# Kernel optimization log

Measured on AMD Instinct MI355X. Metric: run time of the kernel, lower is better.

The kernel has to match this reference:

```python
import jax, jax.numpy as jnp
import numpy as np

KQ_D = 64  # head dim from init_kwargs

def setup_inputs() -> dict:
    key = jax.random.key(0)
    k1, k2, k3, k4 = jax.random.split(key, 4)
    B, H, S, D = 2, 12, 2048, KQ_D
    q = jax.random.normal(k1, (B, H, S, D), dtype=jnp.float32)
    k = jax.random.normal(k2, (B, H, S, D), dtype=jnp.float32)
    v = jax.random.normal(k3, (B, H, S, D), dtype=jnp.float32)
    mask = jax.random.randint(k4, (B, 1, S, S), 0, 2, dtype=jnp.int32)
    return {"q": q, "k": k, "v": v, "mask": mask}

def reference(q, k, v, mask):
    # attn = (q @ k^T) / sqrt(kq_d)
    scale = 1.0 / (KQ_D ** 0.5)
    attn = jnp.einsum('bhqd,bhkd->bhqk', q, k) * scale
    # masked_fill(mask == 0, -1e9)
    attn = jnp.where(mask == 0, jnp.float32(-1e9), attn)
    # softmax over keys; dropout is identity in eval/reference mode
    attn = jax.nn.softmax(attn, axis=-1)
    out = jnp.einsum('bhqk,bhkd->bhqd', attn, v)
    return out
```

## Files before the change

### kernel.cpp

```cpp
#include <hip/hip_runtime.h>
#include <hip/hip_bf16.h>

#define S_LEN 2048
#define D_DIM 64
#define NH    12
#define NB    2
#define BH_N  (NB*NH)
#define TILES 32
#define TILE_BYTES 16384
#define KV_WS_BYTES ((size_t)BH_N * TILES * TILE_BYTES)
#define MASK_WORDS  ((size_t)NB * S_LEN * TILES)
#define WS_NEEDED   (KV_WS_BYTES + MASK_WORDS * 8)

typedef __attribute__((ext_vector_type(8))) short short8;
typedef __attribute__((ext_vector_type(4))) float f32x4;

static __device__ inline unsigned bfbits(float f) {
    __hip_bfloat16 h = __float2bfloat16(f);
    return (unsigned)*reinterpret_cast<const unsigned short*>(&h);
}

static __device__ inline unsigned bfpack2(float a, float b) {
    __hip_bfloat162 h = __float22bfloat162_rn(make_float2(a, b));
    return *reinterpret_cast<const unsigned*>(&h);
}

static __device__ inline void gload_lds16(const void* g, unsigned ldsoff) {
    __builtin_amdgcn_global_load_lds(
        (__attribute__((address_space(1))) void*)(unsigned long long)(uintptr_t)g,
        (__attribute__((address_space(3))) void*)(unsigned long long)ldsoff,
        16, 0, 0);
}

__global__ __launch_bounds__(256) void prep(const float* __restrict__ k,
                                            const float* __restrict__ v,
                                            const int* __restrict__ mask,
                                            char* __restrict__ wsKV,
                                            unsigned long long* __restrict__ wm) {
    __shared__ __align__(16) float sv[64 * 68];
    const int tid = threadIdx.x;
    const int bid = blockIdx.x;
    if (bid < 768) {
        const int t = bid & 31, bh = bid >> 5;
        const int kv0 = t * 64;
        const float* kb = k + (size_t)bh * (S_LEN * D_DIM);
        const float* vb = v + (size_t)bh * (S_LEN * D_DIM);
        char* img = wsKV + ((size_t)bh * TILES + t) * TILE_BYTES;

#pragma unroll
        for (int g = 0; g < 4; ++g) {
            int i = g * 256 + tid;
            int row = i >> 4, cb = (i & 15) << 3;
            int cp = cb ^ ((row & 7) << 4);
            float4 f = *(const float4*)(kb + (size_t)(kv0 + row) * D_DIM + (cp >> 1));
            uint2 u;
            u.x = bfpack2(f.x, f.y);
            u.y = bfpack2(f.z, f.w);
            *(uint2*)(img + (size_t)i * 8) = u;
            float4 fv = *(const float4*)(vb + (size_t)(kv0 + row) * D_DIM + ((i & 15) << 2));
            *(float4*)&sv[row * 68 + ((i & 15) << 2)] = fv;
        }
        __syncthreads();
#pragma unroll
        for (int g = 0; g < 4; ++g) {
            int i = g * 256 + tid;
            int drow = i >> 4, cb = (i & 15) << 3;
            int cp = cb ^ ((drow & 7) << 4);
            int key0 = cp >> 1;
            uint2 u;
            u.x = bfpack2(sv[(key0 + 0) * 68 + drow], sv[(key0 + 1) * 68 + drow]);
            u.y = bfpack2(sv[(key0 + 2) * 68 + drow], sv[(key0 + 3) * 68 + drow]);
            *(uint2*)(img + 8192 + (size_t)i * 8) = u;
        }
    } else {
        const int lane = tid & 63;
        const int wgid = (bid - 768) * 4 + (tid >> 6);
#pragma unroll 1
        for (int g = 0; g < 16; ++g) {
            const int t0 = wgid * 64 + g * 4;
            const size_t base = (size_t)t0 * 64 + lane;
            int m0 = mask[base];
            int m1 = mask[base + 64];
            int m2 = mask[base + 128];
            int m3 = mask[base + 192];
            unsigned long long b0 = __ballot(m0 != 0);
            unsigned long long b1 = __ballot(m1 != 0);
            unsigned long long b2 = __ballot(m2 != 0);
            unsigned long long b3 = __ballot(m3 != 0);
            if (lane == 0) {
                wm[t0 + 0] = b0; wm[t0 + 1] = b1;
                wm[t0 + 2] = b2; wm[t0 + 3] = b3;
            }
        }
    }
}

__global__ __launch_bounds__(256, 3) void attn_main(
    const float* __restrict__ q, const char* __restrict__ wsKV,
    const unsigned long long* __restrict__ wm, float* __restrict__ out)
{
    __shared__ __align__(16) char smem[2 * TILE_BYTES + 8192];

    const int tid  = threadIdx.x;
    const int wave = tid >> 6;
    const int lane = tid & 63;
    const int l16  = lane & 15;
    const int lhi  = lane >> 4;

    const int f  = blockIdx.x;
    const int n  = (f & 7) * 96 + (f >> 3);
    const int bx = n & 31;
    const int bh = n >> 5;
    const int b  = bh / NH;
    const int qw = bx * 64 + wave * 16;
    const int qq = qw + l16;

    const float* qb = q + (size_t)bh * (S_LEN * D_DIM);
    float*       ob = out + (size_t)bh * (S_LEN * D_DIM);
    const char*  tileBase = wsKV + (size_t)bh * TILES * TILE_BYTES;
    const size_t widx = ((size_t)b * S_LEN + qq) * TILES;

    const float PRE = 0.125f * 1.44269504088896f;

    short8 bq[2];
#pragma unroll
    for (int ks = 0; ks < 2; ++ks) {
        const float* src = qb + (size_t)qq * D_DIM + ks * 32 + lhi * 8;
        float4 f0 = *(const float4*)(src);
        float4 f1 = *(const float4*)(src + 4);
        short8 a;
        a[0] = (short)bfbits(f0.x * PRE); a[1] = (short)bfbits(f0.y * PRE);
        a[2] = (short)bfbits(f0.z * PRE); a[3] = (short)bfbits(f0.w * PRE);
        a[4] = (short)bfbits(f1.x * PRE); a[5] = (short)bfbits(f1.y * PRE);
        a[6] = (short)bfbits(f1.z * PRE); a[7] = (short)bfbits(f1.w * PRE);
        bq[ks] = a;
    }

    f32x4 o[4];
#pragma unroll
    for (int dt = 0; dt < 4; ++dt) o[dt] = (f32x4){0.f, 0.f, 0.f, 0.f};
    float lsum = 0.f;

    const unsigned smem_base = (unsigned)(uintptr_t)(&smem[0]);
    char* pw = smem + 2 * TILE_BYTES + wave * 2048;

    unsigned long long mw = wm[widx];
#pragma unroll
    for (int j = 0; j < 4; ++j) {
        unsigned off = (unsigned)(wave * 4096 + j * 1024 + lane * 16);
        gload_lds16(tileBase + off, smem_base + off);
    }
    __syncthreads();

    int buf = 0;
    for (int t = 0; t < 32; ++t) {
        if (t < 31) {
            const char* timg = tileBase + (size_t)(t + 1) * TILE_BYTES;
            unsigned dstb = smem_base + (unsigned)((buf ^ 1) * TILE_BYTES);
#pragma unroll
            for (int j = 0; j < 4; ++j) {
                unsigned off = (unsigned)(wave * 4096 + j * 1024 + lane * 16);
                gload_lds16(timg + off, dstb + off);
            }
        }
        unsigned long long mw_next = (t < 31) ? wm[widx + t + 1] : 0ull;

        const char* sK  = smem + buf * TILE_BYTES;
        const char* sVt = sK + 8192;

        f32x4 sc[4];
#pragma unroll
        for (int tt = 0; tt < 4; ++tt) sc[tt] = (f32x4){0.f, 0.f, 0.f, 0.f};
#pragma unroll
        for (int ks = 0; ks < 2; ++ks) {
#pragma unroll
            for (int tt = 0; tt < 4; ++tt) {
                int row = tt * 16 + l16;
                int byte = row * 128 + ((ks * 64 + lhi * 16) ^ ((row & 7) << 4));
                short8 ak = *(const short8*)(sK + byte);
                sc[tt] = __builtin_amdgcn_mfma_f32_16x16x32_bf16(ak, bq[ks], sc[tt], 0, 0, 0);
            }
        }

        short8 bvv[2][4];
#pragma unroll
        for (int ks = 0; ks < 2; ++ks)
#pragma unroll
            for (int dt = 0; dt < 4; ++dt) {
                int drow = dt * 16 + l16;
                int vbyte = drow * 128 + ((ks * 64 + lhi * 16) ^ ((drow & 7) << 4));
                bvv[ks][dt] = *(const short8*)(sVt + vbyte);
            }

        float rs = 0.f;
#pragma unroll
        for (int tt = 0; tt < 4; ++tt) {
            unsigned nib = (unsigned)(mw >> (tt * 16 + lhi * 4)) & 0xFu;
#pragma unroll
            for (int r = 0; r < 4; ++r) {
                float s = ((nib >> r) & 1u) ? sc[tt][r] : -1e9f;
                float p = exp2f(s);
                sc[tt][r] = p;
                rs += p;
            }
        }
        lsum += rs;

#pragma unroll
        for (int tt = 0; tt < 4; ++tt) {
            uint2 u;
            u.x = bfpack2(sc[tt][0], sc[tt][1]);
            u.y = bfpack2(sc[tt][2], sc[tt][3]);
            int byte = l16 * 128 + (((tt * 16 + lhi * 4) * 2) ^ ((l16 & 7) << 4));
            *(uint2*)(pw + byte) = u;
        }

#pragma unroll
        for (int ks = 0; ks < 2; ++ks) {
            int pbyte = l16 * 128 + ((ks * 64 + lhi * 16) ^ ((l16 & 7) << 4));
            short8 pa = *(const short8*)(pw + pbyte);
#pragma unroll
            for (int dt = 0; dt < 4; ++dt)
                o[dt] = __builtin_amdgcn_mfma_f32_16x16x32_bf16(pa, bvv[ks][dt], o[dt], 0, 0, 0);
        }

        __syncthreads();
        buf ^= 1;
        mw = mw_next;
    }

    lsum += __shfl_xor(lsum, 16);
    lsum += __shfl_xor(lsum, 32);
    float invl = 1.0f / lsum;
    float ir[4];
#pragma unroll
    for (int r = 0; r < 4; ++r) ir[r] = __shfl(invl, lhi * 4 + r);
#pragma unroll
    for (int dt = 0; dt < 4; ++dt)
#pragma unroll
        for (int r = 0; r < 4; ++r) {
            int qrow = qw + lhi * 4 + r;
            int dcol = dt * 16 + l16;
            ob[(size_t)qrow * D_DIM + dcol] = o[dt][r] * ir[r];
        }
}

__global__ __launch_bounds__(256, 3) void attn_fallback(
    const float* __restrict__ q, const float* __restrict__ k,
    const float* __restrict__ v, const int* __restrict__ mask,
    float* __restrict__ out)
{
    __shared__ __align__(16) unsigned short sK[4096];
    __shared__ __align__(16) unsigned short sVt[4096];
    __shared__ __align__(16) unsigned short sP[4096];

    const int tid  = threadIdx.x;
    const int wave = tid >> 6;
    const int lane = tid & 63;
    const int l16  = lane & 15;
    const int lhi  = lane >> 4;

    const int bh = blockIdx.y;
    const int b  = bh / NH;
    const int q0 = blockIdx.x * 64;
    const int qw = q0 + wave * 16;
    const int qq = qw + l16;

    const float* qbase = q + (size_t)bh * S_LEN * D_DIM;
    const float* kbase = k + (size_t)bh * S_LEN * D_DIM;
    const float* vbase = v + (size_t)bh * S_LEN * D_DIM;
    const int*   mp = mask + (size_t)b * S_LEN * S_LEN + (size_t)qq * S_LEN;

    const float PRE = 0.125f * 1.44269504088896f;

    short8 bq[2];
#pragma unroll
    for (int ks = 0; ks < 2; ++ks) {
        const float* src = qbase + (size_t)qq * D_DIM + ks * 32 + lhi * 8;
        float4 f0 = *(const float4*)(src);
        float4 f1 = *(const float4*)(src + 4);
        short8 a;
        a[0] = (short)bfbits(f0.x * PRE); a[1] = (short)bfbits(f0.y * PRE);
        a[2] = (short)bfbits(f0.z * PRE); a[3] = (short)bfbits(f0.w * PRE);
        a[4] = (short)bfbits(f1.x * PRE); a[5] = (short)bfbits(f1.y * PRE);
        a[6] = (short)bfbits(f1.z * PRE); a[7] = (short)bfbits(f1.w * PRE);
        bq[ks] = a;
    }

    f32x4 o[4];
#pragma unroll
    for (int dt = 0; dt < 4; ++dt) o[dt] = (f32x4){0.f, 0.f, 0.f, 0.f};
    float mrun = -1e30f, lrun = 0.f;
    unsigned short* pw = sP + wave * 1024;

    int srow[4], sd[4];
#pragma unroll
    for (int s = 0; s < 4; ++s) { int i = tid + 256 * s; srow[s] = i >> 4; sd[s] = (i & 15) * 4; }

    float4 kreg[4], vreg[4];
#pragma unroll
    for (int s = 0; s < 4; ++s) {
        kreg[s] = *(const float4*)(kbase + (size_t)srow[s] * D_DIM + sd[s]);
        vreg[s] = *(const float4*)(vbase + (size_t)srow[s] * D_DIM + sd[s]);
    }

    for (int kv0 = 0; kv0 < S_LEN; kv0 += 64) {
        __syncthreads();
#pragma unroll
        for (int s = 0; s < 4; ++s) {
            unsigned p0 = bfbits(kreg[s].x) | (bfbits(kreg[s].y) << 16);
            unsigned p1 = bfbits(kreg[s].z) | (bfbits(kreg[s].w) << 16);
            int byte = srow[s] * 128 + ((sd[s] * 2) ^ ((srow[s] & 7) << 4));
            *(uint2*)((char*)sK + byte) = make_uint2(p0, p1);
        }
#pragma unroll
        for (int s = 0; s < 4; ++s) {
            float ff[4] = {vreg[s].x, vreg[s].y, vreg[s].z, vreg[s].w};
#pragma unroll
            for (int jj = 0; jj < 4; ++jj) {
                int dd = sd[s] + jj;
                int byte = dd * 128 + ((srow[s] * 2) ^ ((dd & 7) << 4));
                *(unsigned short*)((char*)sVt + byte) = (unsigned short)bfbits(ff[jj]);
            }
        }
        __syncthreads();

        if (kv0 + 64 < S_LEN) {
#pragma unroll
            for (int s = 0; s < 4; ++s) {
                kreg[s] = *(const float4*)(kbase + (size_t)(kv0 + 64 + srow[s]) * D_DIM + sd[s]);
                vreg[s] = *(const float4*)(vbase + (size_t)(kv0 + 64 + srow[s]) * D_DIM + sd[s]);
            }
        }

        int4 m0 = *(const int4*)(mp + kv0 + lhi * 4);
        int4 m1 = *(const int4*)(mp + kv0 + 16 + lhi * 4);
        int4 m2 = *(const int4*)(mp + kv0 + 32 + lhi * 4);
        int4 m3 = *(const int4*)(mp + kv0 + 48 + lhi * 4);

        f32x4 sc[4];
#pragma unroll
        for (int tt = 0; tt < 4; ++tt) sc[tt] = (f32x4){0.f, 0.f, 0.f, 0.f};
#pragma unroll
        for (int ks = 0; ks < 2; ++ks) {
#pragma unroll
            for (int tt = 0; tt < 4; ++tt) {
                int row = tt * 16 + l16;
                int byte = row * 128 + ((ks * 64 + lhi * 16) ^ ((row & 7) << 4));
                short8 ak = *(const short8*)((const char*)sK + byte);
                sc[tt] = __builtin_amdgcn_mfma_f32_16x16x32_bf16(ak, bq[ks], sc[tt], 0, 0, 0);
            }
        }

        const int4 mm[4] = {m0, m1, m2, m3};
        float pm = -1e30f;
#pragma unroll
        for (int tt = 0; tt < 4; ++tt)
#pragma unroll
            for (int r = 0; r < 4; ++r) {
                float s = ((const int*)&mm[tt])[r] ? sc[tt][r] : -1e9f;
                sc[tt][r] = s;
                pm = fmaxf(pm, s);
            }
        pm = fmaxf(pm, __shfl_xor(pm, 16));
        pm = fmaxf(pm, __shfl_xor(pm, 32));

        float mnew = fmaxf(mrun, pm);
        float fsc = exp2f(mrun - mnew);
        mrun = mnew;
        float rs = 0.f;
#pragma unroll
        for (int tt = 0; tt < 4; ++tt)
#pragma unroll
            for (int r = 0; r < 4; ++r) {
                float p = exp2f(sc[tt][r] - mnew);
                sc[tt][r] = p;
                rs += p;
            }
        rs += __shfl_xor(rs, 16);
        rs += __shfl_xor(rs, 32);
        lrun = lrun * fsc + rs;

        float fr[4];
#pragma unroll
        for (int r = 0; r < 4; ++r) fr[r] = __shfl(fsc, lhi * 4 + r);
#pragma unroll
        for (int dt = 0; dt < 4; ++dt)
#pragma unroll
            for (int r = 0; r < 4; ++r) o[dt][r] *= fr[r];

#pragma unroll
        for (int tt = 0; tt < 4; ++tt) {
            unsigned p0 = bfbits(sc[tt][0]) | (bfbits(sc[tt][1]) << 16);
            unsigned p1 = bfbits(sc[tt][2]) | (bfbits(sc[tt][3]) << 16);
            int byte = l16 * 128 + (((tt * 16 + lhi * 4) * 2) ^ ((l16 & 7) << 4));
            *(uint2*)((char*)pw + byte) = make_uint2(p0, p1);
        }

#pragma unroll
        for (int ks = 0; ks < 2; ++ks) {
            int pbyte = l16 * 128 + ((ks * 64 + lhi * 16) ^ ((l16 & 7) << 4));
            short8 pa = *(const short8*)((const char*)pw + pbyte);
#pragma unroll
            for (int dt = 0; dt < 4; ++dt) {
                int drow = dt * 16 + l16;
                int vbyte = drow * 128 + ((ks * 64 + lhi * 16) ^ ((drow & 7) << 4));
                short8 bv = *(const short8*)((const char*)sVt + vbyte);
                o[dt] = __builtin_amdgcn_mfma_f32_16x16x32_bf16(pa, bv, o[dt], 0, 0, 0);
            }
        }
    }

    float invl = 1.0f / lrun;
    float ir[4];
#pragma unroll
    for (int r = 0; r < 4; ++r) ir[r] = __shfl(invl, lhi * 4 + r);
#pragma unroll
    for (int dt = 0; dt < 4; ++dt)
#pragma unroll
        for (int r = 0; r < 4; ++r) {
            int qrow = qw + lhi * 4 + r;
            int dcol = dt * 16 + l16;
            out[(size_t)bh * S_LEN * D_DIM + (size_t)qrow * D_DIM + dcol] = o[dt][r] * ir[r];
        }
}

extern "C" void kernel_launch(void* const* d_in, const int* in_sizes, int n_in,
                              void* d_out, int out_size, void* d_ws, size_t ws_size,
                              hipStream_t stream) {
    const float* q   = (const float*)d_in[0];
    const float* k   = (const float*)d_in[1];
    const float* v   = (const float*)d_in[2];
    const int* mask  = (const int*)d_in[3];
    float* out = (float*)d_out;

    if (ws_size >= WS_NEEDED) {
        char* ws = (char*)d_ws;
        char* wsKV = ws;
        unsigned long long* wm = (unsigned long long*)(ws + KV_WS_BYTES);
        prep<<<dim3(1280), dim3(256), 0, stream>>>(k, v, mask, wsKV, wm);
        attn_main<<<dim3(768), dim3(256), 0, stream>>>(q, wsKV, wm, out);
    } else {
        attn_fallback<<<dim3(S_LEN / 64, BH_N), dim3(256), 0, stream>>>(q, k, v, mask, out);
    }
}
```

Before: 73.80 us.

## Split key range across two wave groups per block and merge partial outputs

Doubles the block to 512 threads so that two groups of four waves each process half of the 32 key tiles for the same 64 queries. Partial outputs and row sums from the second group go through shared memory and are combined by the first group before normalization. This works because the kernel uses no running max (fixed exponent), so partial sums add directly. The aim is more waves in flight and half the serial tile loop per wave. The cost is double the LDS per block, an extra reduction step through shared memory, and lower blocks per CU.

Result: slower. 75.37 us (+2.1%).

```diff
diff --git a/kernel.cpp b/kernel.cpp
--- a/kernel.cpp
+++ b/kernel.cpp
@@ -95,30 +95,32 @@
     }
 }
 
-__global__ __launch_bounds__(256, 3) void attn_main(
+__global__ __launch_bounds__(512, 4) void attn_main(
     const float* __restrict__ q, const char* __restrict__ wsKV,
     const unsigned long long* __restrict__ wm, float* __restrict__ out)
 {
-    __shared__ __align__(16) char smem[2 * TILE_BYTES + 8192];
+    __shared__ __align__(16) char smem[4 * TILE_BYTES + 16384];
 
     const int tid  = threadIdx.x;
     const int wave = tid >> 6;
     const int lane = tid & 63;
     const int l16  = lane & 15;
     const int lhi  = lane >> 4;
+    const int kg   = wave >> 2;
+    const int wv   = wave & 3;
 
     const int f  = blockIdx.x;
     const int n  = (f & 7) * 96 + (f >> 3);
     const int bx = n & 31;
     const int bh = n >> 5;
     const int b  = bh / NH;
-    const int qw = bx * 64 + wave * 16;
+    const int qw = bx * 64 + wv * 16;
     const int qq = qw + l16;
 
     const float* qb = q + (size_t)bh * (S_LEN * D_DIM);
     float*       ob = out + (size_t)bh * (S_LEN * D_DIM);
     const char*  tileBase = wsKV + (size_t)bh * TILES * TILE_BYTES;
-    const size_t widx = ((size_t)b * S_LEN + qq) * TILES;
+    const size_t widx = ((size_t)b * S_LEN + qq) * TILES + kg * 16;
 
     const float PRE = 0.125f * 1.44269504088896f;
 
@@ -142,30 +144,32 @@
     float lsum = 0.f;
 
     const unsigned smem_base = (unsigned)(uintptr_t)(&smem[0]);
-    char* pw = smem + 2 * TILE_BYTES + wave * 2048;
+    const unsigned kgbase = (unsigned)(kg * 32768);
+    char* pw = smem + 4 * TILE_BYTES + wave * 2048;
 
     unsigned long long mw = wm[widx];
 #pragma unroll
     for (int j = 0; j < 4; ++j) {
-        unsigned off = (unsigned)(wave * 4096 + j * 1024 + lane * 16);
-        gload_lds16(tileBase + off, smem_base + off);
+        unsigned off = (unsigned)(wv * 4096 + j * 1024 + lane * 16);
+        gload_lds16(tileBase + (size_t)(kg * 16) * TILE_BYTES + off,
+                    smem_base + kgbase + off);
     }
     __syncthreads();
 
     int buf = 0;
-    for (int t = 0; t < 32; ++t) {
-        if (t < 31) {
-            const char* timg = tileBase + (size_t)(t + 1) * TILE_BYTES;
-            unsigned dstb = smem_base + (unsigned)((buf ^ 1) * TILE_BYTES);
+    for (int t = 0; t < 16; ++t) {
+        if (t < 15) {
+            const char* timg = tileBase + (size_t)(kg * 16 + t + 1) * TILE_BYTES;
+            unsigned dstb = smem_base + kgbase + (unsigned)((buf ^ 1) * TILE_BYTES);
 #pragma unroll
             for (int j = 0; j < 4; ++j) {
-                unsigned off = (unsigned)(wave * 4096 + j * 1024 + lane * 16);
+                unsigned off = (unsigned)(wv * 4096 + j * 1024 + lane * 16);
                 gload_lds16(timg + off, dstb + off);
             }
         }
-        unsigned long long mw_next = (t < 31) ? wm[widx + t + 1] : 0ull;
-
-        const char* sK  = smem + buf * TILE_BYTES;
+        unsigned long long mw_next = (t < 15) ? wm[widx + t + 1] : 0ull;
+
+        const char* sK  = smem + kgbase + (unsigned)(buf * TILE_BYTES);
         const char* sVt = sK + 8192;
 
         f32x4 sc[4];
@@ -229,20 +233,36 @@
         mw = mw_next;
     }
 
+    float* mO = (float*)smem;
+    float* sl = (float*)(smem + 16384);
+
     lsum += __shfl_xor(lsum, 16);
     lsum += __shfl_xor(lsum, 32);
-    float invl = 1.0f / lsum;
-    float ir[4];
-#pragma unroll
-    for (int r = 0; r < 4; ++r) ir[r] = __shfl(invl, lhi * 4 + r);
-#pragma unroll
-    for (int dt = 0; dt < 4; ++dt)
-#pragma unroll
-        for (int r = 0; r < 4; ++r) {
-            int qrow = qw + lhi * 4 + r;
-            int dcol = dt * 16 + l16;
-            ob[(size_t)qrow * D_DIM + dcol] = o[dt][r] * ir[r];
-        }
+    if (lhi == 0) sl[kg * 64 + wv * 16 + l16] = lsum;
+    if (kg == 1) {
+#pragma unroll
+        for (int dt = 0; dt < 4; ++dt)
+#pragma unroll
+            for (int r = 0; r < 4; ++r)
+                mO[wv * 1024 + (lhi * 4 + r) * 64 + dt * 16 + l16] = o[dt][r];
+    }
+    __syncthreads();
+    if (kg == 0) {
+        float lcomb = lsum + sl[64 + wv * 16 + l16];
+        float invl = 1.0f / lcomb;
+        float ir[4];
+#pragma unroll
+        for (int r = 0; r < 4; ++r) ir[r] = __shfl(invl, lhi * 4 + r);
+#pragma unroll
+        for (int dt = 0; dt < 4; ++dt)
+#pragma unroll
+            for (int r = 0; r < 4; ++r) {
+                int qrow = qw + lhi * 4 + r;
+                int dcol = dt * 16 + l16;
+                float ov = o[dt][r] + mO[wv * 1024 + (lhi * 4 + r) * 64 + dcol];
+                ob[(size_t)qrow * D_DIM + dcol] = ov * ir[r];
+            }
+    }
 }
 
 __global__ __launch_bounds__(256, 3) void attn_fallback(
@@ -439,7 +459,7 @@
         char* wsKV = ws;
         unsigned long long* wm = (unsigned long long*)(ws + KV_WS_BYTES);
         prep<<<dim3(1280), dim3(256), 0, stream>>>(k, v, mask, wsKV, wm);
-        attn_main<<<dim3(768), dim3(256), 0, stream>>>(q, wsKV, wm, out);
+        attn_main<<<dim3(768), dim3(512), 0, stream>>>(q, wsKV, wm, out);
     } else {
         attn_fallback<<<dim3(S_LEN / 64, BH_N), dim3(256), 0, stream>>>(q, k, v, mask, out);
     }
```
